# Performance work log

Measured on AMD Instinct MI355X. Metric: run time of the kernel, lower is better.

The kernel has to match this reference:

```python
import jax, jax.numpy as jnp
import numpy as np

C = 128
HEADS = 4
GROUPS = 8
SHAPE = (1, C, 8, 24, 32)  # N, C, D, H, W
EPS = 1e-5


def setup_inputs() -> dict:
    key = jax.random.key(0)
    ks = jax.random.split(key, 3)
    x = jax.random.normal(ks[0], SHAPE, dtype=jnp.float32)
    mask = jnp.ones((1, 1) + SHAPE[2:], dtype=jnp.float32)
    qkv_w = jax.random.normal(ks[1], (3 * C, C), dtype=jnp.float32) * (1.0 / np.sqrt(C))
    qkv_b = jnp.zeros((3 * C,), dtype=jnp.float32)
    proj_w = jax.random.normal(ks[2], (C, C), dtype=jnp.float32) * (1.0 / np.sqrt(C))
    proj_b = jnp.zeros((C,), dtype=jnp.float32)
    return {
        'x': x, 'mask': mask,
        'gn_w': jnp.ones((C,), dtype=jnp.float32),
        'gn_b': jnp.zeros((C,), dtype=jnp.float32),
        'qkv_w': qkv_w, 'qkv_b': qkv_b,
        'proj_w': proj_w, 'proj_b': proj_b,
    }


def group_norm(x, w, b):
    N, Ch, D, H, W = x.shape
    xg = x.reshape(N, GROUPS, Ch // GROUPS, D, H, W)
    mu = jnp.mean(xg, axis=(2, 3, 4, 5), keepdims=True)
    var = jnp.var(xg, axis=(2, 3, 4, 5), keepdims=True)
    xg = (xg - mu) * jax.lax.rsqrt(var + EPS)
    x = xg.reshape(N, Ch, D, H, W)
    return x * w[None, :, None, None, None] + b[None, :, None, None, None]


def reference(x, mask, gn_w, gn_b, qkv_w, qkv_b, proj_w, proj_b):
    N, Ch, D, H, W = x.shape
    S = D * H * W
    hd = Ch // HEADS  # head dim
    xn = group_norm(x, gn_w, gn_b)
    # 1x1x1 conv == channel GEMM: [N,3C,S]
    qkv = jnp.einsum('ncs,oc->nos', xn.reshape(N, Ch, S), qkv_w) + qkv_b[None, :, None]
    q, k, v = jnp.split(qkv, 3, axis=1)
    # '(h c) s -> h s c' (head-major channel split)
    def to_heads(t):
        return t.reshape(N, HEADS, hd, S).transpose(0, 1, 3, 2)  # n h s c
    q, k, v = to_heads(q), to_heads(k), to_heads(v)
    scale = hd ** -0.5
    scores = jnp.einsum('nhic,nhjc->nhij', q, k) * scale
    probs = jax.nn.softmax(scores, axis=-1)
    out = jnp.einsum('nhij,nhjc->nhic', probs, v)
    # n h s c -> n (h c) s
    out = out.transpose(0, 1, 3, 2).reshape(N, Ch, S)
    out = jnp.einsum('ncs,oc->nos', out, proj_w) + proj_b[None, :, None]
    out = out.reshape(N, Ch, D, H, W)
    return (x + out) * mask, mask
```

## Files before the change

kernel.cpp:

```cpp
#include <hip/hip_runtime.h>
#include <hip/hip_bf16.h>
#include <cstddef>

typedef __bf16 bf16;
typedef __bf16 bf16x4 __attribute__((ext_vector_type(4)));
typedef __bf16 bf16x8 __attribute__((ext_vector_type(8)));
typedef float  f32x4  __attribute__((ext_vector_type(4)));

#define NC   128
#define NS   6144
#define HD   32
#define BKV  64
#define NSPLIT 4
#define NCH  ((NS / NSPLIT) / BKV)
#define GELEMS (16 * NS)
#define QK_SCALE (0.17677669529663689f * 1.4426950408889634f)

__device__ __forceinline__ f32x4 mfma16(bf16x8 a, bf16x8 b, f32x4 c) {
  return __builtin_amdgcn_mfma_f32_16x16x32_bf16(a, b, c, 0, 0, 0);
}
__device__ __forceinline__ void gl16(const bf16* g, void* s) {
  __builtin_amdgcn_global_load_lds((const __attribute__((address_space(1))) void*)g,
                                   (__attribute__((address_space(3))) void*)s, 16, 0, 0);
}
__device__ __forceinline__ int swz(int b) { return b ^ (((b >> 7) & 7) << 4); }
__device__ __forceinline__ unsigned cvtpk(float lo, float hi) {
  unsigned r;
  asm("v_cvt_pk_bf16_f32 %0, %1, %2" : "=v"(r) : "v"(lo), "v"(hi));
  return r;
}
__device__ __forceinline__ bf16x8 mkfrag(unsigned a, unsigned b, unsigned c, unsigned d) {
  union { unsigned u[4]; bf16x8 v; } t;
  t.u[0] = a; t.u[1] = b; t.u[2] = c; t.u[3] = d;
  return t.v;
}

__global__ __launch_bounds__(256) void k_prep_stats(
    const float* __restrict__ qkv_w, const float* __restrict__ qkv_b,
    const float* __restrict__ proj_w, const float* __restrict__ x,
    bf16* __restrict__ wq, bf16* __restrict__ wp, float* __restrict__ bias_s,
    float* __restrict__ partials) {
  int bid = blockIdx.x;
  int tid = threadIdx.x;
  if (bid < 192) {
    int i = bid * 256 + tid;
    if (i < 3 * NC * NC) {
      float v = qkv_w[i];
      if (i < NC * NC) v *= QK_SCALE;
      wq[i] = (bf16)v;
    }
    if (i < NC * NC) wp[i] = (bf16)proj_w[i];
    if (i < 3 * NC) bias_s[i] = qkv_b[i] * ((i < NC) ? QK_SCALE : 1.0f);
    return;
  }
  int b = bid - 192;
  int g = b / 12, chunk = b % 12;
  float sum = 0.f, sq = 0.f;
  #pragma unroll
  for (int k = 0; k < 8; ++k) {
    int f4 = tid + k * 256;
    int c  = f4 >> 7;
    int s4 = f4 & 127;
    const float4 v = ((const float4*)x)[(size_t)(g * 16 + c) * (NS / 4) + chunk * 128 + s4];
    sum += v.x + v.y + v.z + v.w;
    sq  += v.x * v.x + v.y * v.y + v.z * v.z + v.w * v.w;
  }
  #pragma unroll
  for (int off = 32; off; off >>= 1) {
    sum += __shfl_down(sum, off, 64);
    sq  += __shfl_down(sq,  off, 64);
  }
  __shared__ float red[2][4];
  if ((tid & 63) == 0) { red[0][tid >> 6] = sum; red[1][tid >> 6] = sq; }
  __syncthreads();
  if (tid == 0) {
    partials[b * 2 + 0] = red[0][0] + red[0][1] + red[0][2] + red[0][3];
    partials[b * 2 + 1] = red[1][0] + red[1][1] + red[1][2] + red[1][3];
  }
}

__global__ __launch_bounds__(256) void k_qkv(
    const float* __restrict__ x, const float* __restrict__ partials,
    const float* __restrict__ gn_w, const float* __restrict__ gn_b,
    const bf16* __restrict__ wq, const float* __restrict__ bias_s,
    bf16* __restrict__ qg, bf16* __restrict__ kg, bf16* __restrict__ vtg) {
  int ot = blockIdx.x;
  int st = blockIdx.y;
  int tid = threadIdx.x;
  __shared__ __align__(16) char xn[64 * 256];
  __shared__ float swc[NC], sbc[NC];

  if (tid < NC) {
    int g = tid >> 4;
    float sum = 0.f, sq = 0.f;
    #pragma unroll
    for (int i = 0; i < 12; ++i) {
      sum += partials[(g * 12 + i) * 2 + 0];
      sq  += partials[(g * 12 + i) * 2 + 1];
    }
    float mean = sum * (1.0f / GELEMS);
    float var  = sq  * (1.0f / GELEMS) - mean * mean;
    float rstd = rsqrtf(var + 1e-5f);
    float wc = gn_w[tid] * rstd;
    swc[tid] = wc;
    sbc[tid] = gn_b[tid] - mean * wc;
  }
  __syncthreads();

  int s_local = tid & 63;
  int s_glob  = st * 64 + s_local;
  int wk = tid >> 6;
  #pragma unroll
  for (int i = 0; i < 4; ++i) {
    int c0 = (wk * 4 + i) * 8;
    bf16x8 ov;
    #pragma unroll
    for (int j = 0; j < 8; ++j) {
      int c = c0 + j;
      ov[j] = (bf16)(x[(size_t)c * NS + s_glob] * swc[c] + sbc[c]);
    }
    *(bf16x8*)(xn + ((s_local * 256 + c0 * 2) ^ ((s_local & 7) << 4))) = ov;
  }
  __syncthreads();

  int w = tid >> 6, l = tid & 63;
  int lr = l & 15, lg = l >> 4;
  int o_base = ot * 64 + (w >> 1) * 32;
  int sl_base = (w & 1) * 32;
  f32x4 acc[2][2] = {};
  #pragma unroll
  for (int k0 = 0; k0 < NC; k0 += 32) {
    bf16x8 a[2], b[2];
    #pragma unroll
    for (int m = 0; m < 2; ++m)
      a[m] = *(const bf16x8*)(wq + (size_t)(o_base + m * 16 + lr) * NC + k0 + lg * 8);
    #pragma unroll
    for (int n = 0; n < 2; ++n) {
      int row = sl_base + n * 16 + lr;
      b[n] = *(const bf16x8*)(xn + ((row * 256 + (k0 + lg * 8) * 2) ^ ((row & 7) << 4)));
    }
    #pragma unroll
    for (int m = 0; m < 2; ++m)
      #pragma unroll
      for (int n = 0; n < 2; ++n)
        acc[m][n] = mfma16(a[m], b[n], acc[m][n]);
  }
  #pragma unroll
  for (int m = 0; m < 2; ++m)
    #pragma unroll
    for (int n = 0; n < 2; ++n)
      #pragma unroll
      for (int r = 0; r < 4; ++r) {
        int o = o_base + m * 16 + lg * 4 + r;
        int s = st * 64 + sl_base + n * 16 + lr;
        float v = acc[m][n][r] + bias_s[o];
        int rem = o & 127, head = rem >> 5, c32 = rem & 31;
        if (o < NC)          qg[((size_t)head * NS + s) * HD + c32] = (bf16)v;
        else if (o < 2 * NC) kg[((size_t)head * NS + s) * HD + c32] = (bf16)v;
        else {
          int s6 = s & 63;
          int pos = ((s6 & 12) << 2) | (((s6 >> 4) & 3) << 2) | (s6 & 3);
          vtg[((size_t)head * HD + c32) * NS + (s & ~63) + pos] = (bf16)v;
        }
      }
}

__global__ __launch_bounds__(256, 6) void k_attn(
    const bf16* __restrict__ qg, const bf16* __restrict__ kg, const bf16* __restrict__ vtg,
    bf16* __restrict__ accP, float* __restrict__ ml) {
  const int h = blockIdx.y, sp = blockIdx.z;
  const int tid = threadIdx.x;
  const int w = tid >> 6, l = tid & 63;
  const int lr = l & 15, lg = l >> 4;
  const int qrow0 = blockIdx.x * 64 + w * 16;

  __shared__ __align__(16) char kbuf[2][4096];
  __shared__ __align__(16) char vbuf[2][4096];
  const int kswz  = ((lr >> 1) & 7) << 4;
  const int vswz  = (lr & 7) << 4;

  const bf16* qp = qg + (size_t)h * NS * HD;
  const bf16* kp = kg + (size_t)h * NS * HD;
  const bf16* vp = vtg + (size_t)h * HD * NS;

  bf16x8 qf = *(const bf16x8*)(qp + (size_t)(qrow0 + lr) * HD + lg * 8);

  bf16x8 ones;
  #pragma unroll
  for (int j = 0; j < 8; ++j) ones[j] = (bf16)1.0f;

  f32x4 acc0 = {}, acc1 = {};
  f32x4 lacc = {};
  const f32x4 zed = {};
  const int kv_beg = sp * (NS / NSPLIT);

  const int o_st = w * 1024 + (l << 4);
  const int u_st = swz(o_st);
  const bf16* ksrc = kp + (size_t)(kv_beg + (u_st >> 6)) * HD + ((u_st & 63) >> 1);
  const bf16* vsrc = vp + (size_t)(u_st >> 7) * NS + kv_beg + ((u_st & 127) >> 1);

  f32x4 sv[4];
  bf16x8 pf0, pf1;

  auto packP = [&]() {
    float e0[4], e1[4], e2[4], e3[4];
    #pragma unroll
    for (int r = 0; r < 4; ++r) {
      e0[r] = __builtin_amdgcn_exp2f(sv[0][r]);
      e1[r] = __builtin_amdgcn_exp2f(sv[1][r]);
      e2[r] = __builtin_amdgcn_exp2f(sv[2][r]);
      e3[r] = __builtin_amdgcn_exp2f(sv[3][r]);
    }
    pf0 = mkfrag(cvtpk(e0[0], e0[1]), cvtpk(e0[2], e0[3]),
                 cvtpk(e1[0], e1[1]), cvtpk(e1[2], e1[3]));
    pf1 = mkfrag(cvtpk(e2[0], e2[1]), cvtpk(e2[2], e2[3]),
                 cvtpk(e3[0], e3[1]), cvtpk(e3[2], e3[3]));
  };
  auto vfrag = [&](const char* vb, int row, int kk) -> bf16x8 {
    int base = (row + lr) * 128 + lg * 32 + kk * 16;
    return *(const bf16x8*)(vb + (base ^ vswz));
  };

  gl16(ksrc, kbuf[0] + w * 1024);
  gl16(vsrc, vbuf[0] + w * 1024);
  gl16(ksrc + BKV * HD, kbuf[1] + w * 1024);
  __syncthreads();
  #pragma unroll
  for (int t4 = 0; t4 < 4; ++t4) {
    bf16x8 kf = *(const bf16x8*)(kbuf[0] + (((t4 * 16 + lr) * 64 + lg * 16) ^ kswz));
    sv[t4] = mfma16(kf, qf, zed);
  }
  packP();

  for (int t = 0; t < NCH; ++t) {
    const int cur = t & 1, nxt = cur ^ 1;
    const bool hn = (t + 1 < NCH);
    __syncthreads();
    if (hn) gl16(vsrc + (size_t)(t + 1) * BKV, vbuf[nxt] + w * 1024);
    if (t + 2 < NCH) gl16(ksrc + (size_t)(t + 2) * BKV * HD, kbuf[cur] + w * 1024);
    if (hn) {
      #pragma unroll
      for (int t4 = 0; t4 < 4; ++t4) {
        bf16x8 kf = *(const bf16x8*)(kbuf[nxt] + (((t4 * 16 + lr) * 64 + lg * 16) ^ kswz));
        sv[t4] = mfma16(kf, qf, zed);
      }
    }
    {
      const char* vb = vbuf[cur];
      acc0 = mfma16(vfrag(vb, 0,  0), pf0, acc0);
      acc1 = mfma16(vfrag(vb, 16, 0), pf0, acc1);
      lacc = mfma16(ones, pf0, lacc);
      acc0 = mfma16(vfrag(vb, 0,  1), pf1, acc0);
      acc1 = mfma16(vfrag(vb, 16, 1), pf1, acc1);
      lacc = mfma16(ones, pf1, lacc);
    }
    if (hn) packP();
  }

  bf16* base = accP + (size_t)(h * NSPLIT + sp) * 8 * NS * 4;
  size_t qrow = qrow0 + lr;
  bf16x4 o0, o1;
  #pragma unroll
  for (int r = 0; r < 4; ++r) { o0[r] = (bf16)acc0[r]; o1[r] = (bf16)acc1[r]; }
  *(bf16x4*)(base + ((size_t)lg * NS + qrow) * 4)       = o0;
  *(bf16x4*)(base + ((size_t)(4 + lg) * NS + qrow) * 4) = o1;
  if (lg == 0)
    ml[(size_t)(h * NSPLIT + sp) * NS + qrow] = lacc[0];
}

__global__ __launch_bounds__(256) void k_proj(
    const bf16* __restrict__ wp, const bf16* __restrict__ accP, const float* __restrict__ ml,
    const float* __restrict__ proj_b, const float* __restrict__ x,
    const float* __restrict__ mask, float* __restrict__ out) {
  int ot = blockIdx.x;
  int st = blockIdx.y;
  int tid = threadIdx.x;
  __shared__ __align__(16) char at[64 * 256];

  int s_local = tid & 63;
  int s = st * 64 + s_local;
  int wk = tid >> 6;
  if (ot == 0 && tid < 64)
    out[(size_t)NC * NS + st * 64 + tid] = mask[st * 64 + tid];
  #pragma unroll
  for (int i = 0; i < 4; ++i) {
    int c0 = (wk * 4 + i) * 8;
    int h = c0 >> 5;
    float L = 0.f;
    #pragma unroll
    for (int spl = 0; spl < NSPLIT; ++spl)
      L += ml[(size_t)(h * NSPLIT + spl) * NS + s];
    float inv = 1.0f / L;
    float o[8] = {};
    int cg0 = (c0 & 31) >> 2;
    #pragma unroll
    for (int spl = 0; spl < NSPLIT; ++spl) {
      const bf16* bp = accP + ((size_t)((h * NSPLIT + spl) * 8 + cg0) * NS + s) * 4;
      bf16x4 a0 = *(const bf16x4*)(bp);
      bf16x4 a1 = *(const bf16x4*)(bp + (size_t)NS * 4);
      #pragma unroll
      for (int j = 0; j < 4; ++j) {
        o[j]     += (float)a0[j];
        o[4 + j] += (float)a1[j];
      }
    }
    bf16x8 ov;
    #pragma unroll
    for (int j = 0; j < 8; ++j) ov[j] = (bf16)(o[j] * inv);
    *(bf16x8*)(at + ((s_local * 256 + c0 * 2) ^ ((s_local & 7) << 4))) = ov;
  }
  __syncthreads();

  int w = tid >> 6, l = tid & 63;
  int lr = l & 15, lg = l >> 4;
  int o_base = ot * 64 + (w >> 1) * 32;
  int sl_base = (w & 1) * 32;
  f32x4 acc[2][2] = {};
  #pragma unroll
  for (int k0 = 0; k0 < NC; k0 += 32) {
    bf16x8 a[2], b[2];
    #pragma unroll
    for (int m = 0; m < 2; ++m)
      a[m] = *(const bf16x8*)(wp + (size_t)(o_base + m * 16 + lr) * NC + k0 + lg * 8);
    #pragma unroll
    for (int n = 0; n < 2; ++n) {
      int row = sl_base + n * 16 + lr;
      b[n] = *(const bf16x8*)(at + ((row * 256 + (k0 + lg * 8) * 2) ^ ((row & 7) << 4)));
    }
    #pragma unroll
    for (int m = 0; m < 2; ++m)
      #pragma unroll
      for (int n = 0; n < 2; ++n)
        acc[m][n] = mfma16(a[m], b[n], acc[m][n]);
  }
  #pragma unroll
  for (int m = 0; m < 2; ++m)
    #pragma unroll
    for (int n = 0; n < 2; ++n)
      #pragma unroll
      for (int r = 0; r < 4; ++r) {
        int o = o_base + m * 16 + lg * 4 + r;
        int sg = st * 64 + sl_base + n * 16 + lr;
        float v = acc[m][n][r] + proj_b[o] + x[(size_t)o * NS + sg];
        out[(size_t)o * NS + sg] = v * mask[sg];
      }
}

extern "C" void kernel_launch(void* const* d_in, const int* in_sizes, int n_in,
                              void* d_out, int out_size, void* d_ws, size_t ws_size,
                              hipStream_t stream) {
  const float* x      = (const float*)d_in[0];
  const float* mask   = (const float*)d_in[1];
  const float* gn_w   = (const float*)d_in[2];
  const float* gn_b   = (const float*)d_in[3];
  const float* qkv_w  = (const float*)d_in[4];
  const float* qkv_b  = (const float*)d_in[5];
  const float* proj_w = (const float*)d_in[6];
  const float* proj_b = (const float*)d_in[7];

  char* ws = (char*)d_ws;
  float* partials = (float*)(ws + 0);
  float* bias_s   = (float*)(ws + 1024);
  bf16*  wq       = (bf16*)(ws + 4096);
  bf16*  wp       = (bf16*)(ws + 102400);
  bf16*  qg       = (bf16*)(ws + 135168);
  bf16*  kg       = (bf16*)(ws + 1708032);
  bf16*  vtg      = (bf16*)(ws + 3280896);
  bf16*  accP     = (bf16*)(ws + 4853760);
  float* ml       = (float*)(ws + 11145216);
  float* out      = (float*)d_out;

  k_prep_stats<<<288, 256, 0, stream>>>(qkv_w, qkv_b, proj_w, x, wq, wp, bias_s, partials);
  k_qkv       <<<dim3(6, 96), 256, 0, stream>>>(x, partials, gn_w, gn_b, wq, bias_s, qg, kg, vtg);
  k_attn      <<<dim3(96, 4, NSPLIT), 256, 0, stream>>>(qg, kg, vtg, accP, ml);
  k_proj      <<<dim3(2, 96), 256, 0, stream>>>(wp, accP, ml, proj_b, x, mask, out);
}
```

Before: 57.58 us.

## Stage QKV epilogue through LDS for vector stores; halve proj tile size

The QKV GEMM epilogue now writes results into shared memory (reusing the xn buffer) and then issues 16-byte coalesced stores to q/k/v-transposed global buffers, instead of scattered 2-byte stores. Separately, the projection kernel's spatial tile drops from 64 to 32 positions, doubling the grid to 384 blocks so more CUs are occupied. The cost is two extra barriers and an LDS round trip in k_qkv, plus more redundant weight loads across the larger proj grid.

After: 56.76 us. About the same (-1.4%).

```diff
diff --git a/kernel.cpp b/kernel.cpp
--- a/kernel.cpp
+++ b/kernel.cpp
@@ -33,6 +33,9 @@
   union { unsigned u[4]; bf16x8 v; } t;
   t.u[0] = a; t.u[1] = b; t.u[2] = c; t.u[3] = d;
   return t.v;
+}
+__device__ __forceinline__ int vperm(int s6) {
+  return ((s6 & 12) << 2) | (((s6 >> 4) & 3) << 2) | (s6 & 3);
 }
 
 __global__ __launch_bounds__(256) void k_prep_stats(
@@ -145,24 +148,47 @@
       for (int n = 0; n < 2; ++n)
         acc[m][n] = mfma16(a[m], b[n], acc[m][n]);
   }
+
+  __syncthreads();
+  bf16* ot_lds = (bf16*)xn;
+  const bool is_v = (ot >= 4);
   #pragma unroll
   for (int m = 0; m < 2; ++m)
     #pragma unroll
     for (int n = 0; n < 2; ++n)
       #pragma unroll
       for (int r = 0; r < 4; ++r) {
-        int o = o_base + m * 16 + lg * 4 + r;
-        int s = st * 64 + sl_base + n * 16 + lr;
-        float v = acc[m][n][r] + bias_s[o];
-        int rem = o & 127, head = rem >> 5, c32 = rem & 31;
-        if (o < NC)          qg[((size_t)head * NS + s) * HD + c32] = (bf16)v;
-        else if (o < 2 * NC) kg[((size_t)head * NS + s) * HD + c32] = (bf16)v;
-        else {
-          int s6 = s & 63;
-          int pos = ((s6 & 12) << 2) | (((s6 >> 4) & 3) << 2) | (s6 & 3);
-          vtg[((size_t)head * HD + c32) * NS + (s & ~63) + pos] = (bf16)v;
-        }
+        int o_l = (w >> 1) * 32 + m * 16 + lg * 4 + r;
+        int s_l = (w & 1) * 32 + n * 16 + lr;
+        int o = ot * 64 + o_l;
+        bf16 v = (bf16)(acc[m][n][r] + bias_s[o]);
+        if (is_v) ot_lds[o_l * 72 + vperm(s_l)] = v;
+        else      ot_lds[s_l * 72 + o_l]        = v;
       }
+  __syncthreads();
+
+  if (!is_v) {
+    bf16* dst = (ot < 2) ? qg : kg;
+    int head0 = (ot & 1) * 2;
+    int c8 = tid & 3, s_l = tid >> 2;
+    size_t s = (size_t)st * 64 + s_l;
+    #pragma unroll
+    for (int i = 0; i < 2; ++i) {
+      bf16x8 v = *(const bf16x8*)(ot_lds + s_l * 72 + i * 32 + c8 * 8);
+      *(bf16x8*)(dst + ((size_t)(head0 + i) * NS + s) * HD + c8 * 8) = v;
+    }
+  } else {
+    int head0 = (ot - 4) * 2;
+    int c_l = tid >> 2;
+    int head = head0 + (c_l >> 5), c32 = c_l & 31;
+    bf16* drow = vtg + ((size_t)head * HD + c32) * NS + st * 64;
+    #pragma unroll
+    for (int i = 0; i < 2; ++i) {
+      int pos8 = (tid & 3) * 2 + i;
+      bf16x8 v = *(const bf16x8*)(ot_lds + c_l * 72 + pos8 * 8);
+      *(bf16x8*)(drow + pos8 * 8) = v;
+    }
+  }
 }
 
 __global__ __launch_bounds__(256, 6) void k_attn(
@@ -275,16 +301,15 @@
   int ot = blockIdx.x;
   int st = blockIdx.y;
   int tid = threadIdx.x;
-  __shared__ __align__(16) char at[64 * 256];
-
-  int s_local = tid & 63;
-  int s = st * 64 + s_local;
-  int wk = tid >> 6;
-  if (ot == 0 && tid < 64)
-    out[(size_t)NC * NS + st * 64 + tid] = mask[st * 64 + tid];
-  #pragma unroll
-  for (int i = 0; i < 4; ++i) {
-    int c0 = (wk * 4 + i) * 8;
+  __shared__ __align__(16) char at[32 * 256];
+
+  int s_local = tid >> 3;
+  int s = st * 32 + s_local;
+  if (ot == 0 && tid < 32)
+    out[(size_t)NC * NS + st * 32 + tid] = mask[st * 32 + tid];
+  #pragma unroll
+  for (int i = 0; i < 2; ++i) {
+    int c0 = ((tid & 7) * 2 + i) * 8;
     int h = c0 >> 5;
     float L = 0.f;
     #pragma unroll
@@ -314,36 +339,31 @@
   int w = tid >> 6, l = tid & 63;
   int lr = l & 15, lg = l >> 4;
   int o_base = ot * 64 + (w >> 1) * 32;
-  int sl_base = (w & 1) * 32;
-  f32x4 acc[2][2] = {};
+  int sl_base = (w & 1) * 16;
+  f32x4 acc[2] = {};
   #pragma unroll
   for (int k0 = 0; k0 < NC; k0 += 32) {
-    bf16x8 a[2], b[2];
+    bf16x8 a[2], b;
     #pragma unroll
     for (int m = 0; m < 2; ++m)
       a[m] = *(const bf16x8*)(wp + (size_t)(o_base + m * 16 + lr) * NC + k0 + lg * 8);
-    #pragma unroll
-    for (int n = 0; n < 2; ++n) {
-      int row = sl_base + n * 16 + lr;
-      b[n] = *(const bf16x8*)(at + ((row * 256 + (k0 + lg * 8) * 2) ^ ((row & 7) << 4)));
+    {
+      int row = sl_base + lr;
+      b = *(const bf16x8*)(at + ((row * 256 + (k0 + lg * 8) * 2) ^ ((row & 7) << 4)));
     }
     #pragma unroll
     for (int m = 0; m < 2; ++m)
-      #pragma unroll
-      for (int n = 0; n < 2; ++n)
-        acc[m][n] = mfma16(a[m], b[n], acc[m][n]);
+      acc[m] = mfma16(a[m], b, acc[m]);
   }
   #pragma unroll
   for (int m = 0; m < 2; ++m)
     #pragma unroll
-    for (int n = 0; n < 2; ++n)
-      #pragma unroll
-      for (int r = 0; r < 4; ++r) {
-        int o = o_base + m * 16 + lg * 4 + r;
-        int sg = st * 64 + sl_base + n * 16 + lr;
-        float v = acc[m][n][r] + proj_b[o] + x[(size_t)o * NS + sg];
-        out[(size_t)o * NS + sg] = v * mask[sg];
-      }
+    for (int r = 0; r < 4; ++r) {
+      int o = o_base + m * 16 + lg * 4 + r;
+      int sg = st * 32 + sl_base + lr;
+      float v = acc[m][r] + proj_b[o] + x[(size_t)o * NS + sg];
+      out[(size_t)o * NS + sg] = v * mask[sg];
+    }
 }
 
 extern "C" void kernel_launch(void* const* d_in, const int* in_sizes, int n_in,
@@ -373,5 +393,5 @@
   k_prep_stats<<<288, 256, 0, stream>>>(qkv_w, qkv_b, proj_w, x, wq, wp, bias_s, partials);
   k_qkv       <<<dim3(6, 96), 256, 0, stream>>>(x, partials, gn_w, gn_b, wq, bias_s, qg, kg, vtg);
   k_attn      <<<dim3(96, 4, NSPLIT), 256, 0, stream>>>(qg, kg, vtg, accP, ml);
-  k_proj      <<<dim3(2, 96), 256, 0, stream>>>(wp, accP, ml, proj_b, x, mask, out);
-}
+  k_proj      <<<dim3(2, 192), 256, 0, stream>>>(wp, accP, ml, proj_b, x, mask, out);
+}
```
